# Kernel tuning notes

Hardware: AMD Instinct MI355X
Metric: run time of the kernel (lower is better)

## Reference

```python
import math
import jax, jax.numpy as jnp
import numpy as np

EPS = 1e-6
M, B, K, D, DZ = 4, 2048, 32, 256, 128

def setup_inputs() -> dict:
    key = jax.random.key(0)
    ks = jax.random.split(key, 8)
    return {
        "h_nei": jax.random.normal(ks[0], (M, B, K, D), jnp.float32),
        "ew_anc": jax.random.uniform(ks[1], (B, K, M), jnp.float32),
        "view_mask": jnp.ones((B, K, M), jnp.float32),
        "z_anc": jax.random.normal(ks[2], (B, DZ), jnp.float32),
        "lbl_delta": jax.random.normal(ks[3], (B, K, M, D), jnp.float32),
        "lbl_weight": jax.random.normal(ks[4], (B, K, M), jnp.float32) * 0.1,
        "W_Q": jax.random.normal(ks[5], (DZ, D), jnp.float32) / math.sqrt(DZ),
        "W_K": jax.random.normal(ks[6], (M, D, D), jnp.float32) / math.sqrt(D),
        "W_V": jax.random.normal(ks[7], (M, D, D), jnp.float32) / math.sqrt(D),
        "log_vw": jnp.zeros((M,), jnp.float32),
    }

def reference(h_nei, ew_anc, view_mask, z_anc, lbl_delta, lbl_weight, W_Q, W_K, W_V, log_vw):
    # Cross-attention mode (use_query_z=True). Dropout is identity (eval mode).
    d = h_nei.shape[-1]
    Q = z_anc @ W_Q                                            # [B, d]
    Kx = jnp.einsum('mbkd,mde->mbke', h_nei, W_K)              # [M, B, K, d]
    Vx = jnp.einsum('mbkd,mde->mbke', h_nei, W_V)
    Vx = Vx + jnp.moveaxis(lbl_delta, 2, 0)                    # add lbl_delta[:,:,m,:]
    ew = jnp.moveaxis(ew_anc, 2, 0)                            # [M, B, K]
    lw = jnp.moveaxis(lbl_weight, 2, 0)
    vm = jnp.moveaxis(view_mask, 2, 0)
    scores = jnp.einsum('bd,mbkd->mbk', Q, Kx) / math.sqrt(d)
    scores = scores + jnp.log(ew + EPS) + lw
    scores = jnp.where(vm == 0, -1e9, scores)
    attn = jax.nn.softmax(scores, axis=-1)                     # [M, B, K]
    ctx_m = jnp.einsum('mbk,mbkd->mbd', attn, Vx)              # [M, B, d]
    vw = jax.nn.softmax(log_vw)                                # [M]
    return jnp.einsum('m,mbd->bd', vw, ctx_m)                  # [B, d]
```

## Files before the change

### kernel.cpp

```cpp
#include <hip/hip_runtime.h>
#include <hip/hip_bf16.h>
#include <math.h>

#define M_  4
#define B_  2048
#define K_  32
#define D_  256
#define DZ_ 128
#define PAD 68

typedef float f32x4 __attribute__((ext_vector_type(4)));

__global__ void __launch_bounds__(256) k0_wqk(const float* __restrict__ W_Q,
                                              const float* __restrict__ W_K,
                                              float* __restrict__ Wqk) {
    int mz = blockIdx.x;
    int m = mz >> 7, z = mz & 127;
    int d = threadIdx.x;
    __shared__ float wq[D_];
    wq[d] = W_Q[z * D_ + d];
    __syncthreads();
    const float* wk = W_K + (m * D_ + d) * D_;
    float acc = 0.f;
#pragma unroll 8
    for (int e = 0; e < D_; ++e) acc = fmaf(wq[e], wk[e], acc);
    Wqk[(m * DZ_ + z) * D_ + d] = acc;
}

__global__ void __launch_bounds__(256) k1_qk(const float* __restrict__ z_anc,
                                             const float* __restrict__ Wqk,
                                             float* __restrict__ Qk) {
    int m = blockIdx.z;
    int b0 = blockIdx.x * 64, d0 = blockIdx.y * 64;
    int t = threadIdx.x, tx = t & 15, ty = t >> 4;
    __shared__ float As[64 * PAD];
    __shared__ float Bs[64 * PAD];
    float c[4][4] = {};
    for (int kc = 0; kc < DZ_; kc += 64) {
#pragma unroll
        for (int it = 0; it < 4; ++it) {
            int s = it * 256 + t, bi = s >> 4, k4 = (s & 15) * 4;
            *(float4*)&As[bi * PAD + k4] =
                *(const float4*)&z_anc[(b0 + bi) * DZ_ + kc + k4];
        }
#pragma unroll
        for (int it = 0; it < 4; ++it) {
            int s = it * 256 + t, kk = s >> 4, d4 = (s & 15) * 4;
            *(float4*)&Bs[kk * PAD + d4] =
                *(const float4*)&Wqk[(m * DZ_ + kc + kk) * D_ + d0 + d4];
        }
        __syncthreads();
#pragma unroll 4
        for (int kk = 0; kk < 64; ++kk) {
            float a[4];
#pragma unroll
            for (int i = 0; i < 4; ++i) a[i] = As[(ty * 4 + i) * PAD + kk];
            float4 b4 = *(const float4*)&Bs[kk * PAD + tx * 4];
#pragma unroll
            for (int i = 0; i < 4; ++i) {
                c[i][0] = fmaf(a[i], b4.x, c[i][0]);
                c[i][1] = fmaf(a[i], b4.y, c[i][1]);
                c[i][2] = fmaf(a[i], b4.z, c[i][2]);
                c[i][3] = fmaf(a[i], b4.w, c[i][3]);
            }
        }
        __syncthreads();
    }
#pragma unroll
    for (int i = 0; i < 4; ++i) {
        float4 v = make_float4(c[i][0], c[i][1], c[i][2], c[i][3]);
        *(float4*)&Qk[(m * B_ + b0 + ty * 4 + i) * D_ + d0 + tx * 4] = v;
    }
}

__global__ void __launch_bounds__(256) k2_main(
    const float* __restrict__ h_nei, const float* __restrict__ ew_anc,
    const float* __restrict__ vmask, const float* __restrict__ lbl_delta,
    const float* __restrict__ lbl_w, const float* __restrict__ Qk,
    const float* __restrict__ log_vw,
    float* __restrict__ hbar, float* __restrict__ lblp)
{
    int bm = blockIdx.x;
    int b = bm >> 2, m = bm & 3;
    int t = threadIdx.x, w = t >> 6, l = t & 63;
    __shared__ float sc[K_], at[K_];
    __shared__ float partA[4 * D_], partB[4 * D_];

    const float* hb = h_nei + ((size_t)(m * B_ + b)) * (K_ * D_);
    f32x4 h4[8];
#pragma unroll
    for (int i = 0; i < 8; ++i)
        h4[i] = *(const f32x4*)&hb[4 * (i * 256 + t)];

    const float* ldb = lbl_delta + (size_t)b * (K_ * M_ * D_) + m * D_;
    f32x4 ld4[8];
#pragma unroll
    for (int i = 0; i < 8; ++i)
        ld4[i] = *(const f32x4*)&ldb[(size_t)(w * 8 + i) * (M_ * D_) + 4 * l];

    f32x4 q4 = *(const f32x4*)&Qk[(m * B_ + b) * D_ + 4 * l];

    float ew_v = 0.f, lw_v = 0.f, vm_v = 1.f;
    if (t < K_) {
        int idx = (b * K_ + t) * M_ + m;
        ew_v = ew_anc[idx];
        lw_v = lbl_w[idx];
        vm_v = vmask[idx];
    }

    asm volatile("" ::
        "v"(h4[0]), "v"(h4[1]), "v"(h4[2]), "v"(h4[3]),
        "v"(h4[4]), "v"(h4[5]), "v"(h4[6]), "v"(h4[7]),
        "v"(ld4[0]), "v"(ld4[1]), "v"(ld4[2]), "v"(ld4[3]),
        "v"(ld4[4]), "v"(ld4[5]), "v"(ld4[6]), "v"(ld4[7]),
        "v"(q4), "v"(ew_v), "v"(lw_v), "v"(vm_v));

    float lv0 = log_vw[0], lv1 = log_vw[1], lv2 = log_vw[2], lv3 = log_vw[3];
    float mv = fmaxf(fmaxf(lv0, lv1), fmaxf(lv2, lv3));
    float e0 = expf(lv0 - mv), e1 = expf(lv1 - mv),
          e2 = expf(lv2 - mv), e3 = expf(lv3 - mv);
    float vw_m = ((m == 0) ? e0 : (m == 1) ? e1 : (m == 2) ? e2 : e3)
                 / (e0 + e1 + e2 + e3);

#pragma unroll
    for (int i = 0; i < 8; ++i) {
        float v = h4[i].x * q4.x + h4[i].y * q4.y + h4[i].z * q4.z + h4[i].w * q4.w;
        v += __shfl_xor(v, 32); v += __shfl_xor(v, 16); v += __shfl_xor(v, 8);
        v += __shfl_xor(v, 4);  v += __shfl_xor(v, 2);  v += __shfl_xor(v, 1);
        if (l == 0) sc[i * 4 + w] = v;
    }
    __syncthreads();

    if (t < K_) {
        float s = (vm_v == 0.f) ? -1e9f
                                : sc[t] * 0.0625f + logf(ew_v + 1e-6f) + lw_v;
        float mx = s;
        mx = fmaxf(mx, __shfl_xor(mx, 16)); mx = fmaxf(mx, __shfl_xor(mx, 8));
        mx = fmaxf(mx, __shfl_xor(mx, 4));  mx = fmaxf(mx, __shfl_xor(mx, 2));
        mx = fmaxf(mx, __shfl_xor(mx, 1));
        float ee = expf(s - mx);
        float ds = ee;
        ds += __shfl_xor(ds, 16); ds += __shfl_xor(ds, 8); ds += __shfl_xor(ds, 4);
        ds += __shfl_xor(ds, 2);  ds += __shfl_xor(ds, 1);
        at[t] = (ee / ds) * vw_m;
    }
    __syncthreads();

    f32x4 pA = {0.f, 0.f, 0.f, 0.f};
    f32x4 pB = {0.f, 0.f, 0.f, 0.f};
#pragma unroll
    for (int i = 0; i < 8; ++i) {
        float a = at[i * 4 + w];
        pA.x = fmaf(a, h4[i].x, pA.x);
        pA.y = fmaf(a, h4[i].y, pA.y);
        pA.z = fmaf(a, h4[i].z, pA.z);
        pA.w = fmaf(a, h4[i].w, pA.w);
        float g = at[w * 8 + i];
        pB.x = fmaf(g, ld4[i].x, pB.x);
        pB.y = fmaf(g, ld4[i].y, pB.y);
        pB.z = fmaf(g, ld4[i].z, pB.z);
        pB.w = fmaf(g, ld4[i].w, pB.w);
    }
    *(f32x4*)&partA[w * D_ + 4 * l] = pA;
    *(f32x4*)&partB[w * D_ + 4 * l] = pB;
    __syncthreads();

    float hv = partA[t] + partA[D_ + t] + partA[2 * D_ + t] + partA[3 * D_ + t];
    hbar[(size_t)b * (M_ * D_) + m * D_ + t] = hv;
    float lv = partB[t] + partB[D_ + t] + partB[2 * D_ + t] + partB[3 * D_ + t];
    lblp[((size_t)m * B_ + b) * D_ + t] = lv;
}

__global__ void __launch_bounds__(256) k3_gemm(const float* __restrict__ hbar,
                                               const float* __restrict__ W_V,
                                               const float* __restrict__ lblp,
                                               float* __restrict__ out) {
    int b0 = blockIdx.x * 16, e0 = blockIdx.y * 64;
    int t = threadIdx.x, tx = t & 15, ty = t >> 4;
    __shared__ float As[16 * PAD];
    __shared__ float Bs[64 * PAD];
    float c0 = 0.f, c1 = 0.f, c2 = 0.f, c3 = 0.f;
    for (int kc = 0; kc < M_ * D_; kc += 64) {
        {
            int bi = t >> 4, k4 = (t & 15) * 4;
            *(float4*)&As[bi * PAD + k4] =
                *(const float4*)&hbar[(size_t)(b0 + bi) * (M_ * D_) + kc + k4];
        }
#pragma unroll
        for (int it = 0; it < 4; ++it) {
            int s = it * 256 + t, kk = s >> 4, e4 = (s & 15) * 4;
            *(float4*)&Bs[kk * PAD + e4] =
                *(const float4*)&W_V[(size_t)(kc + kk) * D_ + e0 + e4];
        }
        __syncthreads();
#pragma unroll 4
        for (int kk = 0; kk < 64; ++kk) {
            float a0 = As[ty * PAD + kk];
            float4 b4 = *(const float4*)&Bs[kk * PAD + tx * 4];
            c0 = fmaf(a0, b4.x, c0);
            c1 = fmaf(a0, b4.y, c1);
            c2 = fmaf(a0, b4.z, c2);
            c3 = fmaf(a0, b4.w, c3);
        }
        __syncthreads();
    }
    int row = b0 + ty, col = e0 + tx * 4;
    float4 s = make_float4(c0, c1, c2, c3);
#pragma unroll
    for (int mm = 0; mm < 4; ++mm) {
        float4 lp = *(const float4*)&lblp[((size_t)mm * B_ + row) * D_ + col];
        s.x += lp.x; s.y += lp.y; s.z += lp.z; s.w += lp.w;
    }
    *(float4*)&out[(size_t)row * D_ + col] = s;
}

extern "C" void kernel_launch(void* const* d_in, const int* in_sizes, int n_in,
                              void* d_out, int out_size, void* d_ws, size_t ws_size,
                              hipStream_t stream) {
    const float* h_nei     = (const float*)d_in[0];
    const float* ew_anc    = (const float*)d_in[1];
    const float* vmask     = (const float*)d_in[2];
    const float* z_anc     = (const float*)d_in[3];
    const float* lbl_delta = (const float*)d_in[4];
    const float* lbl_w     = (const float*)d_in[5];
    const float* W_Q       = (const float*)d_in[6];
    const float* W_K       = (const float*)d_in[7];
    const float* W_V       = (const float*)d_in[8];
    const float* log_vw    = (const float*)d_in[9];
    float* out = (float*)d_out;

    float* ws   = (float*)d_ws;
    float* Wqk  = ws;
    float* Qk   = Wqk + (M_ * DZ_ * D_);
    float* hbar = Qk + (M_ * B_ * D_);
    float* lblp = hbar + (B_ * M_ * D_);

    k0_wqk<<<M_ * DZ_, 256, 0, stream>>>(W_Q, W_K, Wqk);

    dim3 g1(B_ / 64, D_ / 64, M_);
    k1_qk<<<g1, 256, 0, stream>>>(z_anc, Wqk, Qk);

    k2_main<<<B_ * M_, 256, 0, stream>>>(h_nei, ew_anc, vmask, lbl_delta,
                                         lbl_w, Qk, log_vw, hbar, lblp);

    dim3 g3(B_ / 16, D_ / 64);
    k3_gemm<<<g3, 256, 0, stream>>>(hbar, W_V, lblp, out);
}
```

Measured before the change: 175.1 us.

## Stage h_nei and lbl_delta tiles into LDS via direct global-to-LDS loads

The main attention kernel now loads each block's h_nei and lbl_delta tiles (32x256 floats each) straight into shared memory with global_load_lds instead of holding them in registers. The weighted-sum phase then reads columns from LDS per thread over all 32 neighbours, which removes the cross-wave partial-sum buffers and the extra reduction barrier. This frees VGPRs and simplifies the reduction. In exchange it uses 64 KB of LDS per block, which may limit how many blocks fit on a CU and so reduce latency hiding in this memory-bound kernel.

Measured after the change: 179.1 us. 1.02x slower.

```diff
diff --git a/kernel.cpp b/kernel.cpp
--- a/kernel.cpp
+++ b/kernel.cpp
@@ -8,8 +8,6 @@
 #define D_  256
 #define DZ_ 128
 #define PAD 68
-
-typedef float f32x4 __attribute__((ext_vector_type(4)));
 
 __global__ void __launch_bounds__(256) k0_wqk(const float* __restrict__ W_Q,
                                               const float* __restrict__ W_K,
@@ -73,6 +71,12 @@
     }
 }
 
+__device__ __forceinline__ void gl_lds16(const float* g, float* lds) {
+    __builtin_amdgcn_global_load_lds(
+        (const __attribute__((address_space(1))) void*)g,
+        (__attribute__((address_space(3))) void*)lds, 16, 0, 0);
+}
+
 __global__ void __launch_bounds__(256) k2_main(
     const float* __restrict__ h_nei, const float* __restrict__ ew_anc,
     const float* __restrict__ vmask, const float* __restrict__ lbl_delta,
@@ -83,23 +87,20 @@
     int bm = blockIdx.x;
     int b = bm >> 2, m = bm & 3;
     int t = threadIdx.x, w = t >> 6, l = t & 63;
+    __shared__ float hs[K_ * D_];
+    __shared__ float ls[K_ * D_];
     __shared__ float sc[K_], at[K_];
-    __shared__ float partA[4 * D_], partB[4 * D_];
-
-    const float* hb = h_nei + ((size_t)(m * B_ + b)) * (K_ * D_);
-    f32x4 h4[8];
-#pragma unroll
-    for (int i = 0; i < 8; ++i)
-        h4[i] = *(const f32x4*)&hb[4 * (i * 256 + t)];
-
+
+    const float* hb  = h_nei + ((size_t)(m * B_ + b)) * (K_ * D_);
     const float* ldb = lbl_delta + (size_t)b * (K_ * M_ * D_) + m * D_;
-    f32x4 ld4[8];
-#pragma unroll
-    for (int i = 0; i < 8; ++i)
-        ld4[i] = *(const f32x4*)&ldb[(size_t)(w * 8 + i) * (M_ * D_) + 4 * l];
-
-    f32x4 q4 = *(const f32x4*)&Qk[(m * B_ + b) * D_ + 4 * l];
-
+#pragma unroll
+    for (int j = 0; j < 8; ++j) {
+        int k = w * 8 + j;
+        gl_lds16(hb + k * D_ + 4 * l, hs + k * D_);
+        gl_lds16(ldb + (size_t)k * (M_ * D_) + 4 * l, ls + k * D_);
+    }
+
+    float4 q4 = *(const float4*)&Qk[(m * B_ + b) * D_ + 4 * l];
     float ew_v = 0.f, lw_v = 0.f, vm_v = 1.f;
     if (t < K_) {
         int idx = (b * K_ + t) * M_ + m;
@@ -107,14 +108,6 @@
         lw_v = lbl_w[idx];
         vm_v = vmask[idx];
     }
-
-    asm volatile("" ::
-        "v"(h4[0]), "v"(h4[1]), "v"(h4[2]), "v"(h4[3]),
-        "v"(h4[4]), "v"(h4[5]), "v"(h4[6]), "v"(h4[7]),
-        "v"(ld4[0]), "v"(ld4[1]), "v"(ld4[2]), "v"(ld4[3]),
-        "v"(ld4[4]), "v"(ld4[5]), "v"(ld4[6]), "v"(ld4[7]),
-        "v"(q4), "v"(ew_v), "v"(lw_v), "v"(vm_v));
-
     float lv0 = log_vw[0], lv1 = log_vw[1], lv2 = log_vw[2], lv3 = log_vw[3];
     float mv = fmaxf(fmaxf(lv0, lv1), fmaxf(lv2, lv3));
     float e0 = expf(lv0 - mv), e1 = expf(lv1 - mv),
@@ -122,12 +115,16 @@
     float vw_m = ((m == 0) ? e0 : (m == 1) ? e1 : (m == 2) ? e2 : e3)
                  / (e0 + e1 + e2 + e3);
 
-#pragma unroll
-    for (int i = 0; i < 8; ++i) {
-        float v = h4[i].x * q4.x + h4[i].y * q4.y + h4[i].z * q4.z + h4[i].w * q4.w;
+    __syncthreads();
+
+#pragma unroll
+    for (int j = 0; j < 8; ++j) {
+        int k = w * 8 + j;
+        float4 h4 = *(const float4*)&hs[k * D_ + 4 * l];
+        float v = h4.x * q4.x + h4.y * q4.y + h4.z * q4.z + h4.w * q4.w;
         v += __shfl_xor(v, 32); v += __shfl_xor(v, 16); v += __shfl_xor(v, 8);
         v += __shfl_xor(v, 4);  v += __shfl_xor(v, 2);  v += __shfl_xor(v, 1);
-        if (l == 0) sc[i * 4 + w] = v;
+        if (l == 0) sc[k] = v;
     }
     __syncthreads();
 
@@ -146,29 +143,15 @@
     }
     __syncthreads();
 
-    f32x4 pA = {0.f, 0.f, 0.f, 0.f};
-    f32x4 pB = {0.f, 0.f, 0.f, 0.f};
-#pragma unroll
-    for (int i = 0; i < 8; ++i) {
-        float a = at[i * 4 + w];
-        pA.x = fmaf(a, h4[i].x, pA.x);
-        pA.y = fmaf(a, h4[i].y, pA.y);
-        pA.z = fmaf(a, h4[i].z, pA.z);
-        pA.w = fmaf(a, h4[i].w, pA.w);
-        float g = at[w * 8 + i];
-        pB.x = fmaf(g, ld4[i].x, pB.x);
-        pB.y = fmaf(g, ld4[i].y, pB.y);
-        pB.z = fmaf(g, ld4[i].z, pB.z);
-        pB.w = fmaf(g, ld4[i].w, pB.w);
-    }
-    *(f32x4*)&partA[w * D_ + 4 * l] = pA;
-    *(f32x4*)&partB[w * D_ + 4 * l] = pB;
-    __syncthreads();
-
-    float hv = partA[t] + partA[D_ + t] + partA[2 * D_ + t] + partA[3 * D_ + t];
-    hbar[(size_t)b * (M_ * D_) + m * D_ + t] = hv;
-    float lv = partB[t] + partB[D_ + t] + partB[2 * D_ + t] + partB[3 * D_ + t];
-    lblp[((size_t)m * B_ + b) * D_ + t] = lv;
+    float ah = 0.f, al = 0.f;
+#pragma unroll 8
+    for (int k = 0; k < K_; ++k) {
+        float a = at[k];
+        ah = fmaf(a, hs[k * D_ + t], ah);
+        al = fmaf(a, ls[k * D_ + t], al);
+    }
+    hbar[(size_t)b * (M_ * D_) + m * D_ + t] = ah;
+    lblp[((size_t)m * B_ + b) * D_ + t] = al;
 }
 
 __global__ void __launch_bounds__(256) k3_gemm(const float* __restrict__ hbar,
```
